# Optimization experiments

Hardware: AMD Instinct MI355X
Metric: run time of the kernel (lower is better)

## Reference

```python
import jax, jax.numpy as jnp
import numpy as np

B, T, M, P, N2 = 16, 8192, 128, 128, 128  # N2 = N//2 complex modes

def setup_inputs() -> dict:
    key = jax.random.key(0)
    k1, k2, k3, k4, k5 = jax.random.split(key, 5)
    u = jax.random.normal(k1, (B, T, M), dtype=jnp.float32)
    # log-parametrized Lambda (S5 'log' convention): Lambda = -exp(row0) + 1j*row1
    log_re = jnp.log(jax.random.uniform(k2, (N2,), minval=0.1, maxval=1.0))
    im = jnp.pi * jnp.arange(N2, dtype=jnp.float32)  # HiPPO-like imaginary spread
    Lambda_param = jnp.stack([log_re, im], axis=0).astype(jnp.float32)
    B_param = jax.random.normal(k3, (2, N2, M), dtype=jnp.float32) / np.sqrt(M)
    C_param = jax.random.normal(k4, (2, P, N2), dtype=jnp.float32) / np.sqrt(N2)
    delta = jnp.array([0.01], dtype=jnp.float32)  # default_\u0394
    return {"u": u, "Lambda_param": Lambda_param, "B_param": B_param,
            "C_param": C_param, "delta": delta}

def reference(u, Lambda_param, B_param, C_param, delta):
    # Reconstruct complex continuous-time matrices
    Lam = (-jnp.exp(Lambda_param[0]) + 1j * Lambda_param[1]).astype(jnp.complex64)   # (N2,)
    Bc = (B_param[0] + 1j * B_param[1]).astype(jnp.complex64)                        # (N2, M)
    Cc = (C_param[0] + 1j * C_param[1]).astype(jnp.complex64)                        # (P, N2)
    d = delta[0]
    # ZOH discretization: Lambda_d = exp(Lam*d), Bd = ((Lambda_d - 1)/Lam) * B
    Ld = jnp.exp(Lam * d)                                                            # (N2,)
    Bd = ((Ld - 1.0) / Lam)[:, None] * Bc                                            # (N2, M)
    # Input projection: Bu[b,t,n] = sum_m u[b,t,m] * Bd[n,m]
    Bu = jnp.einsum('btm,nm->btn', u.astype(jnp.complex64), Bd)                      # (B,T,N2)
    # Parallel scan of x_{k+1} = Ld * x_k + Bu_k, x_0 = 0 -> x holds x_1..x_T
    A = jnp.broadcast_to(Ld, Bu.shape)
    def comb(e1, e2):
        a1, b1 = e1
        a2, b2 = e2
        return (a1 * a2, a2 * b1 + b2)
    _, x = jax.lax.associative_scan(comb, (A, Bu), axis=1)                           # (B,T,N2)
    # return_next_y=True: y_k = 2*Re(C x_{k+1})
    y = 2.0 * jnp.real(jnp.einsum('btn,pn->btp', x, Cc))                             # (B,T,P)
    return y
```

## Files before the change

kernel.cpp:

```cpp
#include <hip/hip_runtime.h>
#include <hip/hip_bf16.h>

#define LCH 128
#define NCH 64
#define NCHUNKS 1024

typedef __attribute__((ext_vector_type(8))) short short8v;
typedef __attribute__((ext_vector_type(4))) short short4v;
typedef __attribute__((ext_vector_type(4))) float f32x4;

#define WS_LDINV_RE 0
#define WS_LDINV_IM 16384
#define WS_LDP_RE   32768
#define WS_LDP_IM   49152
#define WS_E_RE     65536
#define WS_E_IM     (65536 + 131072)
#define WS_CIN_RE   (65536 + 262144)
#define WS_CIN_IM   (65536 + 393216)
#define WS_F32_END  (65536 + 524288)
#define WS_WPACK_BYTE  (589824 * 4)
#define WS_CCPACK_BYTE (589824 * 4 + 65536)

__device__ inline unsigned short f2bf(float f) {
    union { float f; unsigned u; } v; v.f = f;
    unsigned r = v.u + 0x7FFF + ((v.u >> 16) & 1);
    return (unsigned short)(r >> 16);
}

__global__ void k0_pows(const float* __restrict__ lp, const float* __restrict__ delta,
                        float* __restrict__ ws) {
    const int r = blockIdx.x;
    const int tid = threadIdx.x;
    const int n = tid & 127;
    const double d = (double)delta[0];
    const double lre = -exp((double)lp[n]);
    const double lim = (double)lp[128 + n];
    const double kk = (double)(r + 1) * d;
    if (tid < 128) {
        const double mag = exp(-lre * kk);
        ws[WS_LDINV_RE + r * 128 + n] = (float)(mag * cos(lim * kk));
        ws[WS_LDINV_IM + r * 128 + n] = (float)(-mag * sin(lim * kk));
    } else {
        const double mag = exp(lre * kk);
        ws[WS_LDP_RE + r * 128 + n] = (float)(mag * cos(lim * kk));
        ws[WS_LDP_IM + r * 128 + n] = (float)(mag * sin(lim * kk));
    }
}

__global__ void k0_wpack(const float* __restrict__ lp, const float* __restrict__ bp,
                         const float* __restrict__ delta, unsigned short* __restrict__ wpack) {
    const int gid = blockIdx.x * 512 + threadIdx.x;
    const int j = gid & 7;
    const int lane = (gid >> 3) & 63;
    const int ks = (gid >> 9) & 3;
    const int ntile = gid >> 11;
    const int np = ntile * 16 + (lane & 15);
    const int m = ks * 32 + ((lane >> 4) & 3) * 8 + j;
    const int n = np & 127;
    const double d = (double)delta[0];
    const double lre = -exp((double)lp[n]);
    const double lim = (double)lp[128 + n];
    const double er = exp(lre * d);
    const double ldr = er * cos(lim * d), ldi = er * sin(lim * d);
    const double nr = ldr - 1.0, ni = ldi;
    const double den = lre * lre + lim * lim;
    const double cr = (nr * lre + ni * lim) / den;
    const double ci = (ni * lre - nr * lim) / den;
    const double br = (double)bp[n * 128 + m];
    const double bi = (double)bp[16384 + n * 128 + m];
    const double v = (np < 128) ? (cr * br - ci * bi) : (cr * bi + ci * br);
    wpack[gid] = f2bf((float)v);
}

__global__ void k0_cpack(const float* __restrict__ cp, unsigned short* __restrict__ ccpack) {
    const int gid = blockIdx.x * 512 + threadIdx.x;
    const int j = gid & 7;
    const int lane = (gid >> 3) & 63;
    const int ks = (gid >> 9) & 7;
    const int ptile = gid >> 12;
    const int p = ptile * 16 + (lane & 15);
    const int k = ks * 32 + ((lane >> 4) & 3) * 8 + j;
    const int n = k >> 1;
    const float v = ((k & 1) == 0) ? 2.0f * cp[p * 128 + n] : -2.0f * cp[16384 + p * 128 + n];
    ccpack[gid] = f2bf(v);
}

__device__ inline void stage_u(const float* __restrict__ uchunk, unsigned short* lds_u) {
    const float4* uf = (const float4*)uchunk;
    const int tid = threadIdx.x;
#pragma unroll
    for (int it = 0; it < 8; ++it) {
        const int f4 = it * 512 + tid;
        const float4 v = uf[f4];
        const int e = f4 * 4;
        const int t = e >> 7;
        const int m = e & 127;
        const int byte = (t * 256 + m * 2) ^ ((t & 7) << 4);
        short4v wv;
        wv[0] = (short)f2bf(v.x); wv[1] = (short)f2bf(v.y);
        wv[2] = (short)f2bf(v.z); wv[3] = (short)f2bf(v.w);
        *(short4v*)((char*)lds_u + byte) = wv;
    }
}

__device__ inline void gemm1(const unsigned short* lds_u, const unsigned short* wpack,
                             int w, int lane, f32x4 acc[8][2]) {
    const short8v* wp = (const short8v*)wpack;
    const int tl = lane & 15;
    const int gq = (lane >> 4) & 3;
#pragma unroll
    for (int ks = 0; ks < 4; ++ks) {
        const short8v b0 = wp[(w * 4 + ks) * 64 + lane];
        const short8v b1 = wp[((8 + w) * 4 + ks) * 64 + lane];
#pragma unroll
        for (int tt = 0; tt < 8; ++tt) {
            const int t = tt * 16 + tl;
            const int byte = (t * 256 + (ks * 32 + gq * 8) * 2) ^ ((t & 7) << 4);
            const short8v a = *(const short8v*)((const char*)lds_u + byte);
            acc[tt][0] = __builtin_amdgcn_mfma_f32_16x16x32_bf16(a, b0, acc[tt][0], 0, 0, 0);
            acc[tt][1] = __builtin_amdgcn_mfma_f32_16x16x32_bf16(a, b1, acc[tt][1], 0, 0, 0);
        }
    }
}

__global__ __launch_bounds__(512) void k1_end(const float* __restrict__ u,
                                              float* __restrict__ ws,
                                              const unsigned short* __restrict__ wpack) {
    __shared__ unsigned short lds_u[16384];
    const int tid = threadIdx.x;
    const int lane = tid & 63;
    const int w = tid >> 6;
    const int g = blockIdx.x;
    const int b = g >> 6;
    const int c = g & 63;
    stage_u(u + (size_t)(b * 8192 + c * 128) * 128, lds_u);
    __syncthreads();
    f32x4 acc[8][2];
#pragma unroll
    for (int i = 0; i < 8; ++i) { acc[i][0] = (f32x4)0.f; acc[i][1] = (f32x4)0.f; }
    gemm1(lds_u, wpack, w, lane, acc);
    const int tl = lane & 15;
    const int gq = (lane >> 4) & 3;
    const int n = w * 16 + tl;
    float er = 0.f, ei = 0.f;
#pragma unroll
    for (int tt = 0; tt < 8; ++tt) {
#pragma unroll
        for (int reg = 0; reg < 4; ++reg) {
            const int r = tt * 16 + gq * 4 + reg;
            const float lir = ws[WS_LDINV_RE + r * 128 + n];
            const float lii = ws[WS_LDINV_IM + r * 128 + n];
            const float br = acc[tt][0][reg], bi = acc[tt][1][reg];
            er += lir * br - lii * bi;
            ei += lir * bi + lii * br;
        }
    }
    er += __shfl_xor(er, 16); ei += __shfl_xor(ei, 16);
    er += __shfl_xor(er, 32); ei += __shfl_xor(ei, 32);
    const float ldr = ws[WS_LDP_RE + 127 * 128 + n];
    const float ldi = ws[WS_LDP_IM + 127 * 128 + n];
    if (gq == 0 && (lane >> 4) == 0) {
        ws[WS_E_RE + g * 128 + n] = ldr * er - ldi * ei;
        ws[WS_E_IM + g * 128 + n] = ldr * ei + ldi * er;
    }
}

__global__ void k2_carry(float* __restrict__ ws) {
    const int idx = blockIdx.x * 256 + threadIdx.x;
    const int b = idx >> 7;
    const int n = idx & 127;
    const float lr = ws[WS_LDP_RE + 127 * 128 + n];
    const float li = ws[WS_LDP_IM + 127 * 128 + n];
    float cr = 0.f, ci = 0.f;
    for (int c = 0; c < NCH; ++c) {
        const int o = (b * NCH + c) * 128 + n;
        ws[WS_CIN_RE + o] = cr;
        ws[WS_CIN_IM + o] = ci;
        const float er = ws[WS_E_RE + o];
        const float ei = ws[WS_E_IM + o];
        const float nr = fmaf(lr, cr, fmaf(-li, ci, er));
        const float ni = fmaf(lr, ci, fmaf(li, cr, ei));
        cr = nr; ci = ni;
    }
}

__global__ __launch_bounds__(512) void k3_main(const float* __restrict__ u,
                                               float* __restrict__ ws,
                                               const unsigned short* __restrict__ wpack,
                                               const unsigned short* __restrict__ ccpack,
                                               float* __restrict__ y) {
    __shared__ unsigned short lds[49152];
    unsigned short* lds_u = lds;
    unsigned short* lds_bus = lds + 16384;
    const int tid = threadIdx.x;
    const int lane = tid & 63;
    const int w = tid >> 6;
    const int tl = lane & 15;
    const int gq = (lane >> 4) & 3;
    const int g = blockIdx.x;
    const int b = g >> 6;
    const int c = g & 63;
    const int n = w * 16 + tl;

    stage_u(u + (size_t)(b * 8192 + c * 128) * 128, lds_u);
    __syncthreads();

    f32x4 acc[8][2];
#pragma unroll
    for (int i = 0; i < 8; ++i) { acc[i][0] = (f32x4)0.f; acc[i][1] = (f32x4)0.f; }
    gemm1(lds_u, wpack, w, lane, acc);

#pragma unroll
    for (int tt = 0; tt < 8; ++tt) {
        short4v pr, pi;
#pragma unroll
        for (int reg = 0; reg < 4; ++reg) {
            const int r = tt * 16 + gq * 4 + reg;
            const float lir = ws[WS_LDINV_RE + r * 128 + n];
            const float lii = ws[WS_LDINV_IM + r * 128 + n];
            const float br = acc[tt][0][reg], bi = acc[tt][1][reg];
            pr[reg] = (short)f2bf(lir * br - lii * bi);
            pi[reg] = (short)f2bf(lir * bi + lii * br);
        }
        const int s0 = tt * 16 + gq * 4;
        const int rowr = w * 16 + tl;
        *(short4v*)((char*)lds_bus + ((rowr * 256 + s0 * 2) ^ ((rowr & 7) << 4))) = pr;
        const int rowi = 128 + w * 16 + tl;
        *(short4v*)((char*)lds_bus + ((rowi * 256 + s0 * 2) ^ ((rowi & 7) << 4))) = pi;
    }

    short8v ONES, D0, D1;
#pragma unroll
    for (int j = 0; j < 8; ++j) {
        const int sl = gq * 8 + j;
        ONES[j] = (short)0x3F80;
        D0[j] = (sl <= tl) ? (short)0x3F80 : (short)0;
        D1[j] = (sl <= tl + 16) ? (short)0x3F80 : (short)0;
    }
    f32x4 z[8][2];
#pragma unroll
    for (int i = 0; i < 8; ++i) { z[i][0] = (f32x4)0.f; z[i][1] = (f32x4)0.f; }
#pragma unroll
    for (int ks = 0; ks < 4; ++ks) {
        const int rr = w * 16 + tl;
        const short8v b0 = *(const short8v*)((const char*)lds_bus +
                           ((rr * 256 + (ks * 32 + gq * 8) * 2) ^ ((rr & 7) << 4)));
        const int ri = 128 + w * 16 + tl;
        const short8v b1 = *(const short8v*)((const char*)lds_bus +
                           ((ri * 256 + (ks * 32 + gq * 8) * 2) ^ ((ri & 7) << 4)));
#pragma unroll
        for (int tt = 0; tt < 8; ++tt) {
            if (tt < 2 * ks) continue;
            const short8v a = (tt == 2 * ks) ? D0 : ((tt == 2 * ks + 1) ? D1 : ONES);
            z[tt][0] = __builtin_amdgcn_mfma_f32_16x16x32_bf16(a, b0, z[tt][0], 0, 0, 0);
            z[tt][1] = __builtin_amdgcn_mfma_f32_16x16x32_bf16(a, b1, z[tt][1], 0, 0, 0);
        }
    }
    __syncthreads();

    const float cr = ws[WS_CIN_RE + g * 128 + n];
    const float ci = ws[WS_CIN_IM + g * 128 + n];
#pragma unroll
    for (int tt = 0; tt < 8; ++tt) {
#pragma unroll
        for (int reg = 0; reg < 4; ++reg) {
            const int r = tt * 16 + gq * 4 + reg;
            const float ldr = ws[WS_LDP_RE + r * 128 + n];
            const float ldi = ws[WS_LDP_IM + r * 128 + n];
            const float zr = z[tt][0][reg] + cr;
            const float zi = z[tt][1][reg] + ci;
            const float xr = ldr * zr - ldi * zi;
            const float xi = ldr * zi + ldi * zr;
            const unsigned pack = (unsigned)f2bf(xr) | ((unsigned)f2bf(xi) << 16);
            const int byte = (r * 512 + n * 4) ^ ((r & 7) << 4);
            *(unsigned*)((char*)lds + byte) = pack;
        }
    }
    __syncthreads();

    const short8v* cc = (const short8v*)ccpack;
    f32x4 yac[8];
#pragma unroll
    for (int i = 0; i < 8; ++i) yac[i] = (f32x4)0.f;
#pragma unroll
    for (int ks = 0; ks < 8; ++ks) {
        const short8v bfrg = cc[(w * 8 + ks) * 64 + lane];
#pragma unroll
        for (int tt = 0; tt < 8; ++tt) {
            const int t = tt * 16 + tl;
            const int byte = (t * 512 + (ks * 32 + gq * 8) * 2) ^ ((t & 7) << 4);
            const short8v a = *(const short8v*)((const char*)lds + byte);
            yac[tt] = __builtin_amdgcn_mfma_f32_16x16x32_bf16(a, bfrg, yac[tt], 0, 0, 0);
        }
    }
    const int p = w * 16 + tl;
    float* yrow = y + (size_t)(b * 8192 + c * 128) * 128;
#pragma unroll
    for (int tt = 0; tt < 8; ++tt) {
#pragma unroll
        for (int reg = 0; reg < 4; ++reg) {
            const int t = tt * 16 + gq * 4 + reg;
            yrow[t * 128 + p] = yac[tt][reg];
        }
    }
}

extern "C" void kernel_launch(void* const* d_in, const int* in_sizes, int n_in,
                              void* d_out, int out_size, void* d_ws, size_t ws_size,
                              hipStream_t stream) {
    const float* u     = (const float*)d_in[0];
    const float* lp    = (const float*)d_in[1];
    const float* bp    = (const float*)d_in[2];
    const float* cp    = (const float*)d_in[3];
    const float* delta = (const float*)d_in[4];
    float* y  = (float*)d_out;
    float* ws = (float*)d_ws;
    unsigned short* wpack  = (unsigned short*)((char*)d_ws + WS_WPACK_BYTE);
    unsigned short* ccpack = (unsigned short*)((char*)d_ws + WS_CCPACK_BYTE);

    k0_pows <<<128, 256, 0, stream>>>(lp, delta, ws);
    k0_wpack<<<64, 512, 0, stream>>>(lp, bp, delta, wpack);
    k0_cpack<<<64, 512, 0, stream>>>(cp, ccpack);
    k1_end  <<<NCHUNKS, 512, 0, stream>>>(u, ws, wpack);
    k2_carry<<<8, 256, 0, stream>>>(ws);
    k3_main <<<NCHUNKS, 512, 0, stream>>>(u, ws, wpack, ccpack, y);
}
```

Baseline: 98.83 us.

## Interleave complex workspace as float2, alias LDS buffers, add MFMA priority and occupancy hints

```diff
diff --git a/kernel.cpp b/kernel.cpp
--- a/kernel.cpp
+++ b/kernel.cpp
@@ -9,26 +9,27 @@
 typedef __attribute__((ext_vector_type(4))) short short4v;
 typedef __attribute__((ext_vector_type(4))) float f32x4;
 
-#define WS_LDINV_RE 0
-#define WS_LDINV_IM 16384
-#define WS_LDP_RE   32768
-#define WS_LDP_IM   49152
-#define WS_E_RE     65536
-#define WS_E_IM     (65536 + 131072)
-#define WS_CIN_RE   (65536 + 262144)
-#define WS_CIN_IM   (65536 + 393216)
-#define WS_F32_END  (65536 + 524288)
+#define W2_LDINV 0
+#define W2_LDP   16384
+#define W2_E     32768
+#define W2_CIN   163840
 #define WS_WPACK_BYTE  (589824 * 4)
 #define WS_CCPACK_BYTE (589824 * 4 + 65536)
 
 __device__ inline unsigned short f2bf(float f) {
-    union { float f; unsigned u; } v; v.f = f;
-    unsigned r = v.u + 0x7FFF + ((v.u >> 16) & 1);
-    return (unsigned short)(r >> 16);
+    union { __hip_bfloat16 h; unsigned short u; } v;
+    v.h = __float2bfloat16(f);
+    return v.u;
+}
+__device__ inline short4v pack4(float a, float b, float c, float d) {
+    union { __hip_bfloat162 h2[2]; short4v s4; } pk;
+    pk.h2[0] = __float22bfloat162_rn(make_float2(a, b));
+    pk.h2[1] = __float22bfloat162_rn(make_float2(c, d));
+    return pk.s4;
 }
 
 __global__ void k0_pows(const float* __restrict__ lp, const float* __restrict__ delta,
-                        float* __restrict__ ws) {
+                        float2* __restrict__ ws2) {
     const int r = blockIdx.x;
     const int tid = threadIdx.x;
     const int n = tid & 127;
@@ -38,12 +39,12 @@
     const double kk = (double)(r + 1) * d;
     if (tid < 128) {
         const double mag = exp(-lre * kk);
-        ws[WS_LDINV_RE + r * 128 + n] = (float)(mag * cos(lim * kk));
-        ws[WS_LDINV_IM + r * 128 + n] = (float)(-mag * sin(lim * kk));
+        ws2[W2_LDINV + r * 128 + n] = make_float2((float)(mag * cos(lim * kk)),
+                                                  (float)(-mag * sin(lim * kk)));
     } else {
         const double mag = exp(lre * kk);
-        ws[WS_LDP_RE + r * 128 + n] = (float)(mag * cos(lim * kk));
-        ws[WS_LDP_IM + r * 128 + n] = (float)(mag * sin(lim * kk));
+        ws2[W2_LDP + r * 128 + n] = make_float2((float)(mag * cos(lim * kk)),
+                                                (float)(mag * sin(lim * kk)));
     }
 }
 
@@ -92,14 +93,10 @@
     for (int it = 0; it < 8; ++it) {
         const int f4 = it * 512 + tid;
         const float4 v = uf[f4];
-        const int e = f4 * 4;
-        const int t = e >> 7;
-        const int m = e & 127;
+        const int t = f4 >> 5;
+        const int m = (f4 & 31) * 4;
         const int byte = (t * 256 + m * 2) ^ ((t & 7) << 4);
-        short4v wv;
-        wv[0] = (short)f2bf(v.x); wv[1] = (short)f2bf(v.y);
-        wv[2] = (short)f2bf(v.z); wv[3] = (short)f2bf(v.w);
-        *(short4v*)((char*)lds_u + byte) = wv;
+        *(short4v*)((char*)lds_u + byte) = pack4(v.x, v.y, v.z, v.w);
     }
 }
 
@@ -108,6 +105,7 @@
     const short8v* wp = (const short8v*)wpack;
     const int tl = lane & 15;
     const int gq = (lane >> 4) & 3;
+    __builtin_amdgcn_s_setprio(1);
 #pragma unroll
     for (int ks = 0; ks < 4; ++ks) {
         const short8v b0 = wp[(w * 4 + ks) * 64 + lane];
@@ -121,11 +119,12 @@
             acc[tt][1] = __builtin_amdgcn_mfma_f32_16x16x32_bf16(a, b1, acc[tt][1], 0, 0, 0);
         }
     }
-}
-
-__global__ __launch_bounds__(512) void k1_end(const float* __restrict__ u,
-                                              float* __restrict__ ws,
-                                              const unsigned short* __restrict__ wpack) {
+    __builtin_amdgcn_s_setprio(0);
+}
+
+__global__ __launch_bounds__(512, 4) void k1_end(const float* __restrict__ u,
+                                                 float2* __restrict__ ws2,
+                                                 const unsigned short* __restrict__ wpack) {
     __shared__ unsigned short lds_u[16384];
     const int tid = threadIdx.x;
     const int lane = tid & 63;
@@ -148,50 +147,45 @@
 #pragma unroll
         for (int reg = 0; reg < 4; ++reg) {
             const int r = tt * 16 + gq * 4 + reg;
-            const float lir = ws[WS_LDINV_RE + r * 128 + n];
-            const float lii = ws[WS_LDINV_IM + r * 128 + n];
+            const float2 li = ws2[W2_LDINV + r * 128 + n];
             const float br = acc[tt][0][reg], bi = acc[tt][1][reg];
-            er += lir * br - lii * bi;
-            ei += lir * bi + lii * br;
+            er += li.x * br - li.y * bi;
+            ei += li.x * bi + li.y * br;
         }
     }
     er += __shfl_xor(er, 16); ei += __shfl_xor(ei, 16);
     er += __shfl_xor(er, 32); ei += __shfl_xor(ei, 32);
-    const float ldr = ws[WS_LDP_RE + 127 * 128 + n];
-    const float ldi = ws[WS_LDP_IM + 127 * 128 + n];
-    if (gq == 0 && (lane >> 4) == 0) {
-        ws[WS_E_RE + g * 128 + n] = ldr * er - ldi * ei;
-        ws[WS_E_IM + g * 128 + n] = ldr * ei + ldi * er;
-    }
-}
-
-__global__ void k2_carry(float* __restrict__ ws) {
+    const float2 ld = ws2[W2_LDP + 127 * 128 + n];
+    if (lane < 16) {
+        ws2[W2_E + g * 128 + n] = make_float2(ld.x * er - ld.y * ei,
+                                              ld.x * ei + ld.y * er);
+    }
+}
+
+__global__ void k2_carry(float2* __restrict__ ws2) {
     const int idx = blockIdx.x * 256 + threadIdx.x;
     const int b = idx >> 7;
     const int n = idx & 127;
-    const float lr = ws[WS_LDP_RE + 127 * 128 + n];
-    const float li = ws[WS_LDP_IM + 127 * 128 + n];
+    const float2 l = ws2[W2_LDP + 127 * 128 + n];
     float cr = 0.f, ci = 0.f;
     for (int c = 0; c < NCH; ++c) {
         const int o = (b * NCH + c) * 128 + n;
-        ws[WS_CIN_RE + o] = cr;
-        ws[WS_CIN_IM + o] = ci;
-        const float er = ws[WS_E_RE + o];
-        const float ei = ws[WS_E_IM + o];
-        const float nr = fmaf(lr, cr, fmaf(-li, ci, er));
-        const float ni = fmaf(lr, ci, fmaf(li, cr, ei));
+        ws2[W2_CIN + o] = make_float2(cr, ci);
+        const float2 e = ws2[W2_E + o];
+        const float nr = fmaf(l.x, cr, fmaf(-l.y, ci, e.x));
+        const float ni = fmaf(l.x, ci, fmaf(l.y, cr, e.y));
         cr = nr; ci = ni;
     }
 }
 
-__global__ __launch_bounds__(512) void k3_main(const float* __restrict__ u,
-                                               float* __restrict__ ws,
-                                               const unsigned short* __restrict__ wpack,
-                                               const unsigned short* __restrict__ ccpack,
-                                               float* __restrict__ y) {
-    __shared__ unsigned short lds[49152];
+__global__ __launch_bounds__(512, 4) void k3_main(const float* __restrict__ u,
+                                                  const float2* __restrict__ ws2,
+                                                  const unsigned short* __restrict__ wpack,
+                                                  const unsigned short* __restrict__ ccpack,
+                                                  float* __restrict__ y) {
+    __shared__ unsigned short lds[32768];
     unsigned short* lds_u = lds;
-    unsigned short* lds_bus = lds + 16384;
+    unsigned short* lds_bus = lds;
     const int tid = threadIdx.x;
     const int lane = tid & 63;
     const int w = tid >> 6;
@@ -209,24 +203,26 @@
 #pragma unroll
     for (int i = 0; i < 8; ++i) { acc[i][0] = (f32x4)0.f; acc[i][1] = (f32x4)0.f; }
     gemm1(lds_u, wpack, w, lane, acc);
+    __syncthreads();
 
 #pragma unroll
     for (int tt = 0; tt < 8; ++tt) {
-        short4v pr, pi;
+        float vr[4], vi[4];
 #pragma unroll
         for (int reg = 0; reg < 4; ++reg) {
             const int r = tt * 16 + gq * 4 + reg;
-            const float lir = ws[WS_LDINV_RE + r * 128 + n];
-            const float lii = ws[WS_LDINV_IM + r * 128 + n];
+            const float2 li = ws2[W2_LDINV + r * 128 + n];
             const float br = acc[tt][0][reg], bi = acc[tt][1][reg];
-            pr[reg] = (short)f2bf(lir * br - lii * bi);
-            pi[reg] = (short)f2bf(lir * bi + lii * br);
+            vr[reg] = li.x * br - li.y * bi;
+            vi[reg] = li.x * bi + li.y * br;
         }
         const int s0 = tt * 16 + gq * 4;
         const int rowr = w * 16 + tl;
-        *(short4v*)((char*)lds_bus + ((rowr * 256 + s0 * 2) ^ ((rowr & 7) << 4))) = pr;
+        *(short4v*)((char*)lds_bus + ((rowr * 256 + s0 * 2) ^ ((rowr & 7) << 4))) =
+            pack4(vr[0], vr[1], vr[2], vr[3]);
         const int rowi = 128 + w * 16 + tl;
-        *(short4v*)((char*)lds_bus + ((rowi * 256 + s0 * 2) ^ ((rowi & 7) << 4))) = pi;
+        *(short4v*)((char*)lds_bus + ((rowi * 256 + s0 * 2) ^ ((rowi & 7) << 4))) =
+            pack4(vi[0], vi[1], vi[2], vi[3]);
     }
 
     short8v ONES, D0, D1;
@@ -258,22 +254,21 @@
     }
     __syncthreads();
 
-    const float cr = ws[WS_CIN_RE + g * 128 + n];
-    const float ci = ws[WS_CIN_IM + g * 128 + n];
+    const float2 cin = ws2[W2_CIN + g * 128 + n];
 #pragma unroll
     for (int tt = 0; tt < 8; ++tt) {
 #pragma unroll
         for (int reg = 0; reg < 4; ++reg) {
             const int r = tt * 16 + gq * 4 + reg;
-            const float ldr = ws[WS_LDP_RE + r * 128 + n];
-            const float ldi = ws[WS_LDP_IM + r * 128 + n];
-            const float zr = z[tt][0][reg] + cr;
-            const float zi = z[tt][1][reg] + ci;
-            const float xr = ldr * zr - ldi * zi;
-            const float xi = ldr * zi + ldi * zr;
-            const unsigned pack = (unsigned)f2bf(xr) | ((unsigned)f2bf(xi) << 16);
+            const float2 ld = ws2[W2_LDP + r * 128 + n];
+            const float zr = z[tt][0][reg] + cin.x;
+            const float zi = z[tt][1][reg] + cin.y;
+            const float xr = ld.x * zr - ld.y * zi;
+            const float xi = ld.x * zi + ld.y * zr;
+            union { __hip_bfloat162 h2; unsigned u; } pk;
+            pk.h2 = __float22bfloat162_rn(make_float2(xr, xi));
             const int byte = (r * 512 + n * 4) ^ ((r & 7) << 4);
-            *(unsigned*)((char*)lds + byte) = pack;
+            *(unsigned*)((char*)lds + byte) = pk.u;
         }
     }
     __syncthreads();
@@ -282,6 +277,7 @@
     f32x4 yac[8];
 #pragma unroll
     for (int i = 0; i < 8; ++i) yac[i] = (f32x4)0.f;
+    __builtin_amdgcn_s_setprio(1);
 #pragma unroll
     for (int ks = 0; ks < 8; ++ks) {
         const short8v bfrg = cc[(w * 8 + ks) * 64 + lane];
@@ -293,6 +289,7 @@
             yac[tt] = __builtin_amdgcn_mfma_f32_16x16x32_bf16(a, bfrg, yac[tt], 0, 0, 0);
         }
     }
+    __builtin_amdgcn_s_setprio(0);
     const int p = w * 16 + tl;
     float* yrow = y + (size_t)(b * 8192 + c * 128) * 128;
 #pragma unroll
@@ -314,14 +311,14 @@
     const float* cp    = (const float*)d_in[3];
     const float* delta = (const float*)d_in[4];
     float* y  = (float*)d_out;
-    float* ws = (float*)d_ws;
+    float2* ws2 = (float2*)d_ws;
     unsigned short* wpack  = (unsigned short*)((char*)d_ws + WS_WPACK_BYTE);
     unsigned short* ccpack = (unsigned short*)((char*)d_ws + WS_CCPACK_BYTE);
 
-    k0_pows <<<128, 256, 0, stream>>>(lp, delta, ws);
+    k0_pows <<<128, 256, 0, stream>>>(lp, delta, ws2);
     k0_wpack<<<64, 512, 0, stream>>>(lp, bp, delta, wpack);
     k0_cpack<<<64, 512, 0, stream>>>(cp, ccpack);
-    k1_end  <<<NCHUNKS, 512, 0, stream>>>(u, ws, wpack);
-    k2_carry<<<8, 256, 0, stream>>>(ws);
-    k3_main <<<NCHUNKS, 512, 0, stream>>>(u, ws, wpack, ccpack, y);
-}
+    k1_end  <<<NCHUNKS, 512, 0, stream>>>(u, ws2, wpack);
+    k2_carry<<<8, 256, 0, stream>>>(ws2);
+    k3_main <<<NCHUNKS, 512, 0, stream>>>(u, ws2, wpack, ccpack, y);
+}
```

After: 108.0 us. +9.3%, slower.
